# Optimization experiments

Hardware: AMD Instinct MI355X
Metric: run time of the kernel (lower is better)

Reference implementation:

```python
import jax, jax.numpy as jnp
import numpy as np

B, DP, N = 8, 3, 2048
DM, K = 128, 20
C4 = DM // 4


def _gather(pts, idx):
    # pts: (b, n, c), idx: (b, n, k) -> (b, n, k, c)
    return jax.vmap(lambda p, i: p[i])(pts, idx)


def _bn(x, gamma, beta, eps=1e-5):
    # train-mode BatchNorm1d; x: (b, c, n), stats over (batch, points)
    mu = jnp.mean(x, axis=(0, 2), keepdims=True)
    var = jnp.var(x, axis=(0, 2), keepdims=True)
    return gamma[None, :, None] * (x - mu) * jax.lax.rsqrt(var + eps) + beta[None, :, None]


def setup_inputs() -> dict:
    key = jax.random.key(0)
    ks = iter(jax.random.split(key, 32))

    def U(shape):
        s = 1.0 / np.sqrt(shape[-1])
        return jax.random.uniform(next(ks), shape, jnp.float32, -s, s)

    d = {}
    d['features'] = jax.random.normal(next(ks), (B, DP, N), jnp.float32)
    d['fc1_w'] = U((DM, DP)); d['fc1_b'] = U((DM,))
    d['fc2_w'] = U((DM, DM)); d['fc2_b'] = U((DM,))
    d['bn_g'] = jnp.ones((DM,), jnp.float32); d['bn_b'] = jnp.zeros((DM,), jnp.float32)
    d['fb1_w'] = U((DM, 2 * DP)); d['fb1_b'] = U((DM,))
    d['fb2_w'] = U((DM, DM)); d['fb2_b'] = U((DM,))
    d['fg1_w'] = U((DM, DM)); d['fg1_b'] = U((DM,))
    d['fg2_w'] = U((DM, DM)); d['fg2_b'] = U((DM,))
    d['wq'] = U((DM, DM)); d['wk'] = U((DM, DM)); d['wv'] = U((DM, DM))
    d['sa_qk_w'] = U((C4, DM))  # q_conv and k_conv share this weight
    d['sa_v_w'] = U((DM, DM)); d['sa_v_b'] = U((DM,))
    d['sa_t_w'] = U((DM, DM)); d['sa_t_b'] = U((DM,))
    d['sa_bn_g'] = jnp.ones((DM,), jnp.float32); d['sa_bn_b'] = jnp.zeros((DM,), jnp.float32)
    return d


def reference(features, fc1_w, fc1_b, fc2_w, fc2_b, bn_g, bn_b,
              fb1_w, fb1_b, fb2_w, fb2_b, fg1_w, fg1_b, fg2_w, fg2_b,
              wq, wk, wv, sa_qk_w, sa_v_w, sa_v_b, sa_t_w, sa_t_b,
              sa_bn_g, sa_bn_b):
    x = features  # (b, dp, n)
    # --- kNN: negative squared pairwise distance, top-k largest = nearest ---
    inner = -2.0 * jnp.einsum('bdn,bdm->bnm', x, x)
    xx = jnp.sum(x * x, axis=1)  # (b, n)
    pd = -xx[:, :, None] - inner - xx[:, None, :]  # (b, n, n)
    idx = jax.lax.top_k(pd, K)[1]  # (b, n, K) neighbor indices
    # --- get_graph_feature: gather neighbors, concat (nbr - ctr, ctr) ---
    xt = jnp.transpose(x, (0, 2, 1))  # (b, n, dp)
    nbr = _gather(xt, idx)  # (b, n, K, dp)
    ctr = jnp.broadcast_to(xt[:, :, None, :], nbr.shape)
    kf = jnp.concatenate([nbr - ctr, ctr], axis=-1)  # (b, n, K, 2*dp)
    # fb edge MLP
    kf = jax.nn.relu(kf @ fb1_w.T + fb1_b) @ fb2_w.T + fb2_b  # (b, n, K, DM)
    # --- point-transformer attention ---
    x1 = xt @ fc1_w.T + fc1_b  # (b, n, DM)
    q = x1 @ wq.T
    kg = _gather(x1 @ wk.T, idx)  # (b, n, K, DM)
    vg = _gather(x1 @ wv.T, idx)  # (b, n, K, DM)
    a = q[:, :, None, :] - kg + kf
    a = jax.nn.relu(a @ fg1_w.T + fg1_b) @ fg2_w.T + fg2_b  # fc_gamma
    attn = jax.nn.log_softmax(a / jnp.sqrt(jnp.float32(DM)), axis=-2)  # over K
    res = jnp.einsum('bnkf,bnkf->bnf', attn, vg + kf)  # (b, n, DM)
    res = jnp.transpose(res @ fc2_w.T + fc2_b, (0, 2, 1))  # (b, DM, n)
    res = jax.nn.relu(_bn(res, bn_g, bn_b)) + jnp.transpose(x1, (0, 2, 1))
    # --- SA_Layer: offset self-attention (q and k share weights) ---
    xqk = jnp.einsum('cd,bdn->bcn', sa_qk_w, res)  # (b, C4, n)
    energy = jnp.einsum('bcn,bcm->bnm', xqk, xqk)  # (b, n, n)
    att = jax.nn.softmax(energy, axis=-1)
    att = att / (1e-9 + jnp.sum(att, axis=1, keepdims=True))
    xv = jnp.einsum('cd,bdn->bcn', sa_v_w, res) + sa_v_b[None, :, None]
    xr = jnp.einsum('bcn,bnm->bcm', xv, att)  # x_v @ attention
    xr = jnp.einsum('cd,bdn->bcn', sa_t_w, res - xr) + sa_t_b[None, :, None]
    xr = jax.nn.relu(_bn(xr, sa_bn_g, sa_bn_b))
    out = res + xr  # (b, DM, n)
    return (jnp.transpose(out, (0, 2, 1)), attn)
```

## Files before the change

kernel.cpp:

```cpp
#include <hip/hip_runtime.h>

#define NPTS 16384
#define NB 2048
#define KNN 20

typedef __attribute__((ext_vector_type(4))) float f32x4;
typedef __attribute__((ext_vector_type(8))) short short8;

union U4S8 { uint4 q; short8 s; };
union W4   { unsigned u[4]; short8 s; };

__device__ __forceinline__ unsigned bf16_rne(float v){
    unsigned u = __float_as_uint(v);
    return (u + 0x7fffu + ((u>>16)&1u)) >> 16;
}
__device__ __forceinline__ unsigned cvt_pk_bf16(float a, float b){
    unsigned r;
    asm("v_cvt_pk_bf16_f32 %0, %1, %2" : "=v"(r) : "v"(a), "v"(b));
    return r;
}
__device__ __forceinline__ unsigned pack_hl(float v){
    unsigned h = cvt_pk_bf16(v, v);
    float r = v - __uint_as_float(h << 16);
    unsigned l = cvt_pk_bf16(r, r);
    return __builtin_amdgcn_perm(l, h, 0x05040100u);
}
__device__ __forceinline__ void pack2(float v0, float v1, unsigned& h2, unsigned& l2){
    h2 = cvt_pk_bf16(v0, v1);
    float r0 = v0 - __uint_as_float(h2 << 16);
    float r1 = v1 - __uint_as_float(h2 & 0xffff0000u);
    l2 = cvt_pk_bf16(r0, r1);
}
__device__ __forceinline__ void split_hl(uint4 w0, uint4 w1, short8& hi, short8& lo){
    W4 h, l;
    h.u[0] = __builtin_amdgcn_perm(w0.y, w0.x, 0x05040100u);
    l.u[0] = __builtin_amdgcn_perm(w0.y, w0.x, 0x07060302u);
    h.u[1] = __builtin_amdgcn_perm(w0.w, w0.z, 0x05040100u);
    l.u[1] = __builtin_amdgcn_perm(w0.w, w0.z, 0x07060302u);
    h.u[2] = __builtin_amdgcn_perm(w1.y, w1.x, 0x05040100u);
    l.u[2] = __builtin_amdgcn_perm(w1.y, w1.x, 0x07060302u);
    h.u[3] = __builtin_amdgcn_perm(w1.w, w1.z, 0x05040100u);
    l.u[3] = __builtin_amdgcn_perm(w1.w, w1.z, 0x07060302u);
    hi = h.s; lo = l.s;
}
__device__ __forceinline__ f32x4 e3_mfma(short8 Ah, short8 Al, short8 Bh, short8 Bl){
    f32x4 acc = (f32x4){0.f,0.f,0.f,0.f};
    acc = __builtin_amdgcn_mfma_f32_16x16x32_bf16(Al, Bh, acc, 0,0,0);
    acc = __builtin_amdgcn_mfma_f32_16x16x32_bf16(Ah, Bl, acc, 0,0,0);
    acc = __builtin_amdgcn_mfma_f32_16x16x32_bf16(Ah, Bh, acc, 0,0,0);
    return acc;
}

__global__ void transpose_kernel(const float* in, float* out, int C){
    int gid = blockIdx.x*256 + threadIdx.x;
    if (gid >= 128*C) return;
    int j = gid / C, c = gid - j*C;
    out[gid] = in[c*128 + j];
}

__global__ void pack_bfrag_kernel(const float* w0, const float* w1, const float* w2, unsigned short* out){
    int gid = blockIdx.x*256 + threadIdx.x;
    if (gid >= 3*16384) return;
    int m = gid >> 14, r = gid & 16383;
    const float* W = (m==0)?w0:(m==1)?w1:w2;
    int e = r & 7, lane = (r>>3) & 63, ks = (r>>9)&3, ct = r>>11;
    int c = ct*16 + (lane&15), j = ks*32 + (lane>>4)*8 + e;
    out[gid] = (unsigned short)bf16_rne(W[c*128 + j]);
}

__global__ __launch_bounds__(256) void knn_kernel(const float* feat, int* g_idx){
    __shared__ float sx[2048], sy[2048], sz[2048];
    __shared__ int swin[32*20];
    int tid = threadIdx.x;
    int p0 = blockIdx.x * 32;
    int b = p0 >> 11;
    const float* fb = feat + b*3*2048;
    for (int i = tid; i < 2048; i += 256){ sx[i]=fb[i]; sy[i]=fb[2048+i]; sz[i]=fb[4096+i]; }
    __syncthreads();

    int chunk = tid & 7, pl = tid >> 3;
    int n = (p0 + pl) & 2047;
    double xi = sx[n], yi = sy[n], zi = sz[n];

    const double SENT = __longlong_as_double(0x7FE0000000000000ll);
    double val[20];
#pragma unroll
    for (int k=0;k<20;k++) val[k] = SENT;

    int base = chunk*256;
    for (int ii=0; ii<256; ii++){
        int i = (ii + (chunk<<2)) & 255;
        int j = base + i;
        double dx = (double)sx[j]-xi, dy = (double)sy[j]-yi, dz = (double)sz[j]-zi;
        double d2 = dx*dx + dy*dy + dz*dz;
        long long kb = ((__double_as_longlong(d2) & ~2047ll) | (long long)j) + (1ll<<61);
        double key = __longlong_as_double(kb);
#pragma unroll
        for (int s=19; s>=1; s--)
            val[s] = fmax(val[s-1], fmin(val[s], key));
        val[0] = fmin(val[0], key);
    }

    for (int kk=0; kk<20; kk++){
        double h = val[0];
        h = fmin(h, __shfl_xor(h, 1));
        h = fmin(h, __shfl_xor(h, 2));
        h = fmin(h, __shfl_xor(h, 4));
        if (val[0] == h){
            swin[pl*20 + kk] = (int)(__double_as_longlong(h) & 2047ll);
#pragma unroll
            for (int s=0;s<19;s++) val[s] = val[s+1];
            val[19] = SENT;
        }
    }
    __syncthreads();
    for (int t = tid; t < 640; t += 256)
        g_idx[p0*20 + t] = swin[t];
}

__global__ void x1_kernel(const float* feat, const float* w, const float* bias, float* x1){
    int gid = blockIdx.x*256 + threadIdx.x;
    int p = gid >> 7, c = gid & 127;
    int b = p >> 11, n = p & 2047;
    const float* fb = feat + b*6144 + n;
    float v = bias[c];
    v += w[c*3+0]*fb[0];
    v += w[c*3+1]*fb[2048];
    v += w[c*3+2]*fb[4096];
    x1[gid] = v;
}

__global__ __launch_bounds__(256) void qkv_kernel(const float* x1, const float* wqT, const float* wkT,
                                                  const float* wvT, float* q, float* k1, float* v1){
    __shared__ float sx[16][128];
    int tid = threadIdx.x;
    int p0 = blockIdx.x * 16;
    for (int t = tid; t < 2048; t += 256) sx[t>>7][t&127] = x1[p0*128 + t];
    __syncthreads();
    int cg = tid & 31, pg = tid >> 5, c0 = cg*4;
    float aq[2][4] = {{0,0,0,0},{0,0,0,0}};
    float ak[2][4] = {{0,0,0,0},{0,0,0,0}};
    float av[2][4] = {{0,0,0,0},{0,0,0,0}};
    for (int j=0;j<128;j++){
        float xa = sx[pg][j], xb = sx[pg+8][j];
        float4 wq4 = *(const float4*)&wqT[j*128 + c0];
        float4 wk4 = *(const float4*)&wkT[j*128 + c0];
        float4 wv4 = *(const float4*)&wvT[j*128 + c0];
        const float* wqp = &wq4.x; const float* wkp = &wk4.x; const float* wvp = &wv4.x;
#pragma unroll
        for (int ci=0; ci<4; ci++){
            aq[0][ci] += wqp[ci]*xa; aq[1][ci] += wqp[ci]*xb;
            ak[0][ci] += wkp[ci]*xa; ak[1][ci] += wkp[ci]*xb;
            av[0][ci] += wvp[ci]*xa; av[1][ci] += wvp[ci]*xb;
        }
    }
#pragma unroll
    for (int pp=0; pp<2; pp++){
        int p = p0 + pg + pp*8;
        *(float4*)&q [p*128 + c0] = make_float4(aq[pp][0],aq[pp][1],aq[pp][2],aq[pp][3]);
        *(float4*)&k1[p*128 + c0] = make_float4(ak[pp][0],ak[pp][1],ak[pp][2],ak[pp][3]);
        *(float4*)&v1[p*128 + c0] = make_float4(av[pp][0],av[pp][1],av[pp][2],av[pp][3]);
    }
}

#define ASTR 136
__device__ __forceinline__ void stage_gemm(const unsigned short* bH, const unsigned short* bL,
                                           const unsigned short* wb, int lane, int ct0, f32x4 acc[5][2]){
    short8 bf[2][4];
#pragma unroll
    for (int ci=0; ci<2; ci++)
#pragma unroll
    for (int ks=0; ks<4; ks++){
        U4S8 u; u.q = *(const uint4*)(wb + ((ct0+ci)*4 + ks)*512 + lane*8);
        bf[ci][ks] = u.s;
    }
#pragma unroll
    for (int rt=0; rt<5; rt++)
#pragma unroll
    for (int ci=0; ci<2; ci++)
        acc[rt][ci] = (f32x4){0.f,0.f,0.f,0.f};
    int abase = (lane&15)*ASTR + (lane>>4)*8;
#pragma unroll
    for (int rt=0; rt<5; rt++){
#pragma unroll
        for (int ks=0; ks<4; ks++){
            int off = rt*16*ASTR + ks*32 + abase;
            short8 hi = *(const short8*)(bH + off);
            short8 lo = *(const short8*)(bL + off);
#pragma unroll
            for (int ci=0; ci<2; ci++){
                acc[rt][ci] = __builtin_amdgcn_mfma_f32_16x16x32_bf16(hi, bf[ci][ks], acc[rt][ci], 0,0,0);
                acc[rt][ci] = __builtin_amdgcn_mfma_f32_16x16x32_bf16(lo, bf[ci][ks], acc[rt][ci], 0,0,0);
            }
        }
    }
}

__device__ __forceinline__ void store4(unsigned short* bH, unsigned short* bL,
                                       int r0, int col, unsigned h2, unsigned l2, unsigned h3, unsigned l3){
    bH[(r0+0)*ASTR + col] = (unsigned short)h2;        bL[(r0+0)*ASTR + col] = (unsigned short)l2;
    bH[(r0+1)*ASTR + col] = (unsigned short)(h2>>16);  bL[(r0+1)*ASTR + col] = (unsigned short)(l2>>16);
    bH[(r0+2)*ASTR + col] = (unsigned short)h3;        bL[(r0+2)*ASTR + col] = (unsigned short)l3;
    bH[(r0+3)*ASTR + col] = (unsigned short)(h3>>16);  bL[(r0+3)*ASTR + col] = (unsigned short)(l3>>16);
}

__global__ __launch_bounds__(256, 3) void attn_kernel(
        const float* feat, const int* g_idx, const float* g_q, const float* g_k1, const float* g_v1,
        const unsigned short* wpk,
        const float* fb1w, const float* fb1b, const float* fb2b, const float* fg1b, const float* fg2b,
        float* g_attn, float* g_res){
    __shared__ __align__(16) unsigned short bufH[80*ASTR];
    __shared__ __align__(16) unsigned short bufL[80*ASTR];
    __shared__ float sh_q[512];
    __shared__ float sh_e[80*6];
    __shared__ int   sh_ix[80];
    int tid = threadIdx.x;
    int lane = tid & 63, wave = tid >> 6;
    int bidx = blockIdx.x;
    int blk = ((bidx & 7) << 9) | (bidx >> 3);
    int gp0 = blk * 4;
    int b = gp0 >> 11;
    size_t kvbase = (size_t)b*2048*128;

    sh_q[tid]     = g_q[gp0*128 + tid];
    sh_q[tid+256] = g_q[gp0*128 + tid + 256];
    if (tid < 80){
        int r = tid;
        int nb = g_idx[gp0*20 + r];
        sh_ix[r] = nb;
        int p = (r*205) >> 12;
        int n = (gp0 & 2047) + p;
        const float* fbp = feat + b*6144;
        float cx = fbp[n], cy = fbp[2048+n], cz = fbp[4096+n];
        float nx = fbp[nb], ny = fbp[2048+nb], nz = fbp[4096+nb];
        sh_e[r*6+0] = nx-cx; sh_e[r*6+1] = ny-cy; sh_e[r*6+2] = nz-cz;
        sh_e[r*6+3] = cx;    sh_e[r*6+4] = cy;    sh_e[r*6+5] = cz;
    }
    __syncthreads();

    {
        int c = tid & 127, rh = tid >> 7;
        float w0=fb1w[c*6+0], w1=fb1w[c*6+1], w2=fb1w[c*6+2], w3=fb1w[c*6+3], w4=fb1w[c*6+4], w5=fb1w[c*6+5];
        float bb = fb1b[c];
#pragma unroll
        for (int t=0; t<20; t++){
            int r0 = t*4 + rh, r1 = r0 + 2;
            const float* e0 = &sh_e[r0*6];
            const float* e1 = &sh_e[r1*6];
            float v0 = fmaxf(bb + w0*e0[0]+w1*e0[1]+w2*e0[2]+w3*e0[3]+w4*e0[4]+w5*e0[5], 0.f);
            float v1 = fmaxf(bb + w0*e1[0]+w1*e1[1]+w2*e1[2]+w3*e1[3]+w4*e1[4]+w5*e1[5], 0.f);
            unsigned h2, l2; pack2(v0, v1, h2, l2);
            bufH[r0*ASTR + c] = (unsigned short)h2;       bufL[r0*ASTR + c] = (unsigned short)l2;
            bufH[r1*ASTR + c] = (unsigned short)(h2>>16); bufL[r1*ASTR + c] = (unsigned short)(l2>>16);
        }
    }
    __syncthreads();

    int ct0 = wave*2;
    int colA = ct0*16 + (lane&15);
    int colB = colA + 16;
    int quad = lane >> 4;
    f32x4 acc[5][2];
    float kfr[5][2][4];

    stage_gemm(bufH, bufL, wpk, lane, ct0, acc);
    {
        float bA = fb2b[colA], bB = fb2b[colB];
#pragma unroll
        for (int rt=0; rt<5; rt++)
#pragma unroll
        for (int ci=0; ci<2; ci++){
            int col = ci ? colB : colA;
            float bias = ci ? bB : bA;
            float ain[4];
#pragma unroll
            for (int reg=0; reg<4; reg++){
                int row = rt*16 + quad*4 + reg;
                float kf = acc[rt][ci][reg] + bias;
                kfr[rt][ci][reg] = kf;
                int p = (row*205)>>12;
                int nb = sh_ix[row];
                float kg = g_k1[kvbase + (size_t)nb*128 + col];
                ain[reg] = sh_q[p*128 + col] - kg + kf;
            }
            unsigned h2,l2,h3,l3;
            pack2(ain[0], ain[1], h2, l2);
            pack2(ain[2], ain[3], h3, l3);
            acc[rt][ci][0] = __uint_as_float(h2); acc[rt][ci][1] = __uint_as_float(l2);
            acc[rt][ci][2] = __uint_as_float(h3); acc[rt][ci][3] = __uint_as_float(l3);
        }
    }
    __syncthreads();
#pragma unroll
    for (int rt=0; rt<5; rt++)
#pragma unroll
    for (int ci=0; ci<2; ci++)
        store4(bufH, bufL, rt*16 + quad*4, ci ? colB : colA,
               __float_as_uint(acc[rt][ci][0]), __float_as_uint(acc[rt][ci][1]),
               __float_as_uint(acc[rt][ci][2]), __float_as_uint(acc[rt][ci][3]));
    __syncthreads();

    stage_gemm(bufH, bufL, wpk + 16384, lane, ct0, acc);
    {
        float bA = fg1b[colA], bB = fg1b[colB];
#pragma unroll
        for (int rt=0; rt<5; rt++)
#pragma unroll
        for (int ci=0; ci<2; ci++){
            float bias = ci ? bB : bA;
            float v0 = fmaxf(acc[rt][ci][0] + bias, 0.f);
            float v1 = fmaxf(acc[rt][ci][1] + bias, 0.f);
            float v2 = fmaxf(acc[rt][ci][2] + bias, 0.f);
            float v3 = fmaxf(acc[rt][ci][3] + bias, 0.f);
            unsigned h2,l2,h3,l3;
            pack2(v0, v1, h2, l2);
            pack2(v2, v3, h3, l3);
            acc[rt][ci][0] = __uint_as_float(h2); acc[rt][ci][1] = __uint_as_float(l2);
            acc[rt][ci][2] = __uint_as_float(h3); acc[rt][ci][3] = __uint_as_float(l3);
        }
    }
    __syncthreads();
#pragma unroll
    for (int rt=0; rt<5; rt++)
#pragma unroll
    for (int ci=0; ci<2; ci++)
        store4(bufH, bufL, rt*16 + quad*4, ci ? colB : colA,
               __float_as_uint(acc[rt][ci][0]), __float_as_uint(acc[rt][ci][1]),
               __float_as_uint(acc[rt][ci][2]), __float_as_uint(acc[rt][ci][3]));
    __syncthreads();

    stage_gemm(bufH, bufL, wpk + 32768, lane, ct0, acc);
    {
        const float SCALE = 0.08838834764831845f;
        const float NEGF  = -3e38f;
        float bA = fg2b[colA], bB = fg2b[colB];
#pragma unroll
        for (int ci=0; ci<2; ci++){
            int col = ci ? colB : colA;
            float bias = ci ? bB : bA;
            float lm[5];
#pragma unroll
            for (int rt=0; rt<5; rt++){
#pragma unroll
                for (int reg=0; reg<4; reg++)
                    acc[rt][ci][reg] = (acc[rt][ci][reg] + bias) * SCALE;
                lm[rt] = fmaxf(fmaxf(acc[rt][ci][0], acc[rt][ci][1]), fmaxf(acc[rt][ci][2], acc[rt][ci][3]));
            }
            float m[4];
#pragma unroll
            for (int j=0; j<4; j++){
                float c1 = (j<=quad) ? lm[j]   : NEGF;
                float c2 = (j>=quad) ? lm[j+1] : NEGF;
                m[j] = fmaxf(c1, c2);
                m[j] = fmaxf(m[j], __shfl_xor(m[j], 16));
                m[j] = fmaxf(m[j], __shfl_xor(m[j], 32));
            }
            float mp[5];
            mp[0] = m[0];
            mp[1] = (1<=quad) ? m[1] : m[0];
            mp[2] = (2<=quad) ? m[2] : m[1];
            mp[3] = (3<=quad) ? m[3] : m[2];
            mp[4] = m[3];
            float ls[5];
#pragma unroll
            for (int rt=0; rt<5; rt++){
                float e0 = expf(acc[rt][ci][0] - mp[rt]);
                float e1 = expf(acc[rt][ci][1] - mp[rt]);
                float e2 = expf(acc[rt][ci][2] - mp[rt]);
                float e3 = expf(acc[rt][ci][3] - mp[rt]);
                ls[rt] = (e0 + e1) + (e2 + e3);
            }
            float L[4];
#pragma unroll
            for (int j=0; j<4; j++){
                float c1 = (j<=quad) ? ls[j]   : 0.f;
                float c2 = (j>=quad) ? ls[j+1] : 0.f;
                float S = c1 + c2;
                S += __shfl_xor(S, 16);
                S += __shfl_xor(S, 32);
                L[j] = m[j] + logf(S);
            }
            float Lp[5];
            Lp[0] = L[0];
            Lp[1] = (1<=quad) ? L[1] : L[0];
            Lp[2] = (2<=quad) ? L[2] : L[1];
            Lp[3] = (3<=quad) ? L[3] : L[2];
            Lp[4] = L[3];
            float pv[5];
#pragma unroll
            for (int rt=0; rt<5; rt++){
                float pacc = 0.f;
#pragma unroll
                for (int reg=0; reg<4; reg++){
                    int row = rt*16 + quad*4 + reg;
                    float at = acc[rt][ci][reg] - Lp[rt];
                    g_attn[(size_t)(gp0*20 + row)*128 + col] = at;
                    int nb = sh_ix[row];
                    float vv = g_v1[kvbase + (size_t)nb*128 + col];
                    pacc += at * (vv + kfr[rt][ci][reg]);
                }
                pv[rt] = pacc;
            }
#pragma unroll
            for (int j=0; j<4; j++){
                float c1 = (j<=quad) ? pv[j]   : 0.f;
                float c2 = (j>=quad) ? pv[j+1] : 0.f;
                float P = c1 + c2;
                P += __shfl_xor(P, 16);
                P += __shfl_xor(P, 32);
                pv[j] = P;
            }
            float rv = (quad==0) ? pv[0] : (quad==1) ? pv[1] : (quad==2) ? pv[2] : pv[3];
            g_res[(size_t)(gp0 + quad)*128 + col] = rv;
        }
    }
}

__global__ __launch_bounds__(256) void lin_kernel(const float* X, const float* WT, const float* bias, float* Y){
    __shared__ float sx[16][128];
    int tid = threadIdx.x;
    int p0 = blockIdx.x * 16;
    for (int t = tid; t < 2048; t += 256) sx[t>>7][t&127] = X[p0*128 + t];
    __syncthreads();
    int cg = tid & 31, pg = tid >> 5, c0 = cg*4;
    float a[2][4] = {{0,0,0,0},{0,0,0,0}};
    for (int j=0;j<128;j++){
        float xa = sx[pg][j], xb = sx[pg+8][j];
        float4 w4 = *(const float4*)&WT[j*128 + c0];
        const float* wp = &w4.x;
#pragma unroll
        for (int ci=0;ci<4;ci++){ a[0][ci] += wp[ci]*xa; a[1][ci] += wp[ci]*xb; }
    }
    float4 bv = *(const float4*)&bias[c0];
    const float* bp = &bv.x;
#pragma unroll
    for (int pp=0;pp<2;pp++){
        int p = p0 + pg + pp*8;
        *(float4*)&Y[p*128+c0] = make_float4(a[pp][0]+bp[0], a[pp][1]+bp[1], a[pp][2]+bp[2], a[pp][3]+bp[3]);
    }
}

__global__ __launch_bounds__(256) void l6_kernel(const float* Xa, const float* Xb, const float* WT,
                                                 const float* bias, float* Y){
    __shared__ float sx[16][128];
    int tid = threadIdx.x;
    int p0 = blockIdx.x * 16;
    for (int t = tid; t < 2048; t += 256) sx[t>>7][t&127] = Xa[p0*128 + t] - Xb[p0*128 + t];
    __syncthreads();
    int cg = tid & 31, pg = tid >> 5, c0 = cg*4;
    float a[2][4] = {{0,0,0,0},{0,0,0,0}};
    for (int j=0;j<128;j++){
        float xa = sx[pg][j], xb = sx[pg+8][j];
        float4 w4 = *(const float4*)&WT[j*128 + c0];
        const float* wp = &w4.x;
#pragma unroll
        for (int ci=0;ci<4;ci++){ a[0][ci] += wp[ci]*xa; a[1][ci] += wp[ci]*xb; }
    }
    float4 bv = *(const float4*)&bias[c0];
    const float* bp = &bv.x;
#pragma unroll
    for (int pp=0;pp<2;pp++){
        int p = p0 + pg + pp*8;
        *(float4*)&Y[p*128+c0] = make_float4(a[pp][0]+bp[0], a[pp][1]+bp[1], a[pp][2]+bp[2], a[pp][3]+bp[3]);
    }
}

__global__ __launch_bounds__(256) void l5_kernel(const float* X, const float* WvT, const float* vb,
                                                 const float* WqkT, unsigned* xvt_pk, unsigned* xqk_pk){
    __shared__ float sx[16][128];
    int tid = threadIdx.x;
    int p0 = blockIdx.x * 16;
    for (int t = tid; t < 2048; t += 256) sx[t>>7][t&127] = X[p0*128 + t];
    __syncthreads();
    int cg = tid & 31, pg = tid >> 5, c0 = cg*4;
    {
        float a[2][4] = {{0,0,0,0},{0,0,0,0}};
        for (int j=0;j<128;j++){
            float xa = sx[pg][j], xb = sx[pg+8][j];
            float4 w4 = *(const float4*)&WvT[j*128 + c0];
            const float* wp = &w4.x;
#pragma unroll
            for (int ci=0;ci<4;ci++){ a[0][ci] += wp[ci]*xa; a[1][ci] += wp[ci]*xb; }
        }
        float4 bv = *(const float4*)&vb[c0];
        const float* bp = &bv.x;
#pragma unroll
        for (int pp=0;pp<2;pp++){
            int p = p0 + pg + pp*8;
            int bb = p >> 11, n = p & 2047;
            unsigned* dst = xvt_pk + ((size_t)(bb*64 + (n>>5)))*4096 + (n&31);
#pragma unroll
            for (int ci=0;ci<4;ci++) dst[(c0+ci)*32] = pack_hl(a[pp][ci] + bp[ci]);
        }
    }
    if (cg < 8){
        int cq = cg*4;
        float a[2][4] = {{0,0,0,0},{0,0,0,0}};
        for (int j=0;j<128;j++){
            float xa = sx[pg][j], xb = sx[pg+8][j];
            float4 w4 = *(const float4*)&WqkT[j*32 + cq];
            const float* wp = &w4.x;
#pragma unroll
            for (int ci=0;ci<4;ci++){ a[0][ci] += wp[ci]*xa; a[1][ci] += wp[ci]*xb; }
        }
#pragma unroll
        for (int pp=0;pp<2;pp++){
            int p = p0 + pg + pp*8;
            uint4 w;
            w.x = pack_hl(a[pp][0]); w.y = pack_hl(a[pp][1]);
            w.z = pack_hl(a[pp][2]); w.w = pack_hl(a[pp][3]);
            *(uint4*)&xqk_pk[p*32 + cq] = w;
        }
    }
}

__global__ void bn_stats_kernel(const float* X, float* sums){
    int tid = threadIdx.x;
    int c = tid & 127, half = tid >> 7;
    int r0 = blockIdx.x*128 + half*64;
    float s = 0.f, sq = 0.f;
    for (int r = r0; r < r0+64; r++){
        float v = X[r*128 + c];
        s += v; sq += v*v;
    }
    atomicAdd(&sums[c], s);
    atomicAdd(&sums[128+c], sq);
}

__global__ void bn1_apply_kernel(const float* res2, const float* x1, const float* sums,
                                 const float* g, const float* beta, float* sres){
    int gid = blockIdx.x*256 + threadIdx.x;
    int c = gid & 127;
    float mu = sums[c] * (1.0f/16384.f);
    float var = sums[128+c] * (1.0f/16384.f) - mu*mu;
    float inv = 1.0f / sqrtf(var + 1e-5f);
    float y = g[c]*(res2[gid]-mu)*inv + beta[c];
    sres[gid] = fmaxf(y, 0.f) + x1[gid];
}

__global__ void final_kernel(const float* sres, const float* xr2, const float* sums,
                             const float* g, const float* beta, float* out0){
    int gid = blockIdx.x*256 + threadIdx.x;
    int c = gid & 127;
    float mu = sums[c] * (1.0f/16384.f);
    float var = sums[128+c] * (1.0f/16384.f) - mu*mu;
    float inv = 1.0f / sqrtf(var + 1e-5f);
    float y = g[c]*(xr2[gid]-mu)*inv + beta[c];
    out0[gid] = sres[gid] + fmaxf(y, 0.f);
}

__global__ __launch_bounds__(256) void sa_stats_kernel(const unsigned* xqk_pk, float* rm, float* irs){
    int tid = threadIdx.x;
    int lane = tid & 63, wave = tid >> 6;
    int b = blockIdx.x & 7;
    int i0 = (blockIdx.x >> 3) * 64 + wave*16;
    const unsigned* qb = xqk_pk + (size_t)b*2048*32;
    int quad = lane >> 4, l15 = lane & 15;
    const unsigned* ap = qb + (i0 + l15)*32 + quad*8;
    uint4 a0 = *(const uint4*)ap, a1 = *(const uint4*)(ap+4);
    short8 Ah, Al; split_hl(a0, a1, Ah, Al);

    float m[4] = {-3e38f,-3e38f,-3e38f,-3e38f};
    for (int jt=0; jt<128; jt++){
        const unsigned* bp = qb + (jt*16 + l15)*32 + quad*8;
        uint4 b0 = *(const uint4*)bp, b1 = *(const uint4*)(bp+4);
        short8 Bh, Bl; split_hl(b0,b1,Bh,Bl);
        f32x4 e = (f32x4){0.f,0.f,0.f,0.f};
        e = __builtin_amdgcn_mfma_f32_16x16x32_bf16(Ah, Bh, e, 0,0,0);
#pragma unroll
        for (int r=0;r<4;r++) m[r] = fmaxf(m[r], e[r]);
    }
#pragma unroll
    for (int mk=1; mk<16; mk<<=1)
#pragma unroll
        for (int r=0;r<4;r++) m[r] = fmaxf(m[r], __shfl_xor(m[r], mk));

    float s[4] = {0.f,0.f,0.f,0.f};
    for (int jt=0; jt<128; jt++){
        const unsigned* bp = qb + (jt*16 + l15)*32 + quad*8;
        uint4 b0 = *(const uint4*)bp, b1 = *(const uint4*)(bp+4);
        short8 Bh, Bl; split_hl(b0,b1,Bh,Bl);
        f32x4 e = e3_mfma(Ah,Al,Bh,Bl);
#pragma unroll
        for (int r=0;r<4;r++) s[r] += expf(e[r]-m[r]);
    }
#pragma unroll
    for (int mk=1; mk<16; mk<<=1)
#pragma unroll
        for (int r=0;r<4;r++) s[r] += __shfl_xor(s[r], mk);
    if (l15 == 0){
#pragma unroll
        for (int r=0;r<4;r++){
            int row = i0 + quad*4 + r;
            rm[b*2048+row]  = m[r];
            irs[b*2048+row] = 1.0f/s[r];
        }
    }
}

#define SXV_STR 36
#define ATT_STR 36
#define NSPLIT 4
__global__ __launch_bounds__(256) void sa_xr_part_kernel(const unsigned* xqk_pk, const unsigned* xvt_pk,
                                                         const float* rm, const float* irs,
                                                         float* part, float* cspart){
    __shared__ __align__(16) unsigned sxv[128*SXV_STR];
    __shared__ __align__(16) unsigned attT[32*ATT_STR];
    __shared__ float scs[2][2][16];
    int tid = threadIdx.x;
    int lane = tid & 63, wave = tid >> 6;
    int quad = lane >> 4, l15 = lane & 15;
    int bid = blockIdx.x;
    int b   = bid & 7;
    int rest = bid >> 3;
    int ns  = rest >> 6;
    int mt  = rest & 63;
    int m0 = mt*32;
    int rt = wave >> 1, ct = wave & 1;
    const unsigned* qb = xqk_pk + (size_t)b*2048*32;

    short8 Bmh, Bml;
    {
        const unsigned* bp = qb + (m0 + ct*16 + l15)*32 + quad*8;
        uint4 b0 = *(const uint4*)bp, b1 = *(const uint4*)(bp+4);
        split_hl(b0,b1,Bmh,Bml);
    }
    f32x4 acc[4];
#pragma unroll
    for (int cc=0;cc<4;cc++) acc[cc] = (f32x4){0.f,0.f,0.f,0.f};
    float cs_acc = 0.f;

    int ch0 = ns*16;
    for (int ci16=0; ci16<16; ci16++){
        int chunk = ch0 + ci16;
        int n0 = chunk*32;
        __syncthreads();
        const unsigned* src = xvt_pk + ((size_t)(b*64 + chunk))*4096;
#pragma unroll
        for (int it=0; it<4; it++){
            int u = tid + it*256;
            int c = u >> 3, part_ = u & 7;
            *(uint4*)&sxv[c*SXV_STR + part_*4] = *(const uint4*)(src + u*4);
        }
        const unsigned* ap = qb + (n0 + rt*16 + l15)*32 + quad*8;
        uint4 a0 = *(const uint4*)ap, a1 = *(const uint4*)(ap+4);
        short8 Ah, Al; split_hl(a0,a1,Ah,Al);
        f32x4 e = e3_mfma(Ah,Al,Bmh,Bml);
#pragma unroll
        for (int r=0;r<4;r++){
            int rowg = b*2048 + n0 + rt*16 + quad*4 + r;
            float att = expf(e[r] - rm[rowg]) * irs[rowg];
            cs_acc += att;
            attT[(ct*16+l15)*ATT_STR + rt*16 + quad*4 + r] = pack_hl(att);
        }
        __syncthreads();
        const unsigned* arp = attT + (ct*16+l15)*ATT_STR + quad*8;
        uint4 aa0 = *(const uint4*)arp, aa1 = *(const uint4*)(arp+4);
        short8 Aph, Apl; split_hl(aa0,aa1,Aph,Apl);
#pragma unroll
        for (int cc=0; cc<4; cc++){
            int c0 = (rt*4 + cc)*16;
            const unsigned* xp = &sxv[(c0 + l15)*SXV_STR + quad*8];
            uint4 x0 = *(const uint4*)xp, x1 = *(const uint4*)(xp+4);
            short8 Xh, Xl; split_hl(x0,x1,Xh,Xl);
            acc[cc] = __builtin_amdgcn_mfma_f32_16x16x32_bf16(Apl, Xh, acc[cc], 0,0,0);
            acc[cc] = __builtin_amdgcn_mfma_f32_16x16x32_bf16(Aph, Xl, acc[cc], 0,0,0);
            acc[cc] = __builtin_amdgcn_mfma_f32_16x16x32_bf16(Aph, Xh, acc[cc], 0,0,0);
        }
    }
    cs_acc += __shfl_xor(cs_acc, 16);
    cs_acc += __shfl_xor(cs_acc, 32);
    if (lane < 16) scs[ct][rt][lane] = cs_acc;
    __syncthreads();
    if (tid < 32)
        cspart[(size_t)(ns*8 + b)*2048 + m0 + tid] = scs[tid>>4][0][tid&15] + scs[tid>>4][1][tid&15];
#pragma unroll
    for (int cc=0; cc<4; cc++){
        int c0 = (rt*4 + cc)*16;
#pragma unroll
        for (int r=0;r<4;r++){
            int mloc = ct*16 + quad*4 + r;
            part[((size_t)(ns*8 + b)*2048 + m0 + mloc)*128 + c0 + l15] = acc[cc][r];
        }
    }
}

__global__ void sa_combine_kernel(const float* part, const float* cspart, float* xr){
    int gid = blockIdx.x*256 + threadIdx.x;
    int bm = gid >> 7;
    float cs = cspart[bm] + cspart[bm+16384] + cspart[bm+2*16384] + cspart[bm+3*16384];
    float v  = part[gid] + part[gid+2097152] + part[gid+2*2097152] + part[gid+3*2097152];
    xr[gid] = v * (1.0f/(1e-9f + cs));
}

extern "C" void kernel_launch(void* const* d_in, const int* in_sizes, int n_in,
                              void* d_out, int out_size, void* d_ws, size_t ws_size,
                              hipStream_t stream){
    (void)in_sizes; (void)n_in; (void)out_size; (void)ws_size;
    const float* feat = (const float*)d_in[0];
    const float* fc1w = (const float*)d_in[1];  const float* fc1b = (const float*)d_in[2];
    const float* fc2w = (const float*)d_in[3];  const float* fc2b = (const float*)d_in[4];
    const float* bng  = (const float*)d_in[5];  const float* bnb  = (const float*)d_in[6];
    const float* fb1w = (const float*)d_in[7];  const float* fb1b = (const float*)d_in[8];
    const float* fb2w = (const float*)d_in[9];  const float* fb2b = (const float*)d_in[10];
    const float* fg1w = (const float*)d_in[11]; const float* fg1b = (const float*)d_in[12];
    const float* fg2w = (const float*)d_in[13]; const float* fg2b = (const float*)d_in[14];
    const float* wq   = (const float*)d_in[15]; const float* wk   = (const float*)d_in[16];
    const float* wv   = (const float*)d_in[17];
    const float* saqk = (const float*)d_in[18];
    const float* savw = (const float*)d_in[19]; const float* savb = (const float*)d_in[20];
    const float* satw = (const float*)d_in[21]; const float* satb = (const float*)d_in[22];
    const float* sabng= (const float*)d_in[23]; const float* sabnb= (const float*)d_in[24];

    float* out0 = (float*)d_out;
    float* out1 = out0 + 2097152;

    char* ws = (char*)d_ws;
    size_t off = 0;
    auto A = [&](size_t bytes)->char*{
        char* r = ws + off;
        off = (off + bytes + 255) & ~(size_t)255;
        return r;
    };
    const size_t PBUF = (size_t)NPTS*128*4;
    int*      g_idx  = (int*)A((size_t)NPTS*KNN*4);
    float*    g_x1   = (float*)A(PBUF);
    float*    g_q    = (float*)A(PBUF);
    float*    g_k1   = (float*)A(PBUF);
    float*    g_v1   = (float*)A(PBUF);
    float*    g_res  = (float*)A(PBUF);
    float*    g_res2 = (float*)A(PBUF);
    float*    g_sres = (float*)A(PBUF);
    float*    g_xr   = (float*)A(PBUF);
    float*    g_xr2  = (float*)A(PBUF);
    unsigned* g_xvt_pk = (unsigned*)A((size_t)NPTS*128*4);
    unsigned* g_xqk_pk = (unsigned*)A((size_t)NPTS*32*4);
    float*    g_rm   = (float*)A((size_t)NPTS*4);
    float*    g_rs   = (float*)A((size_t)NPTS*4);
    float*    g_stats= (float*)A((size_t)512*4);
    unsigned short* g_wpk = (unsigned short*)A((size_t)3*16384*2);
    float*    g_wqT  = (float*)A(65536);
    float*    g_wkT  = (float*)A(65536);
    float*    g_wvT  = (float*)A(65536);
    float*    g_fc2T = (float*)A(65536);
    float*    g_savT = (float*)A(65536);
    float*    g_satT = (float*)A(65536);
    float*    g_sqkT = (float*)A(16384);

    float* bn1s = g_stats;
    float* bn2s = g_stats + 256;

    float* g_part   = g_q;
    float* g_cspart = g_res2;

    hipMemsetAsync(g_stats, 0, (size_t)512*4, stream);

    pack_bfrag_kernel<<<192, 256, 0, stream>>>(fb2w, fg1w, fg2w, g_wpk);
    transpose_kernel<<<64, 256, 0, stream>>>(wq,   g_wqT, 128);
    transpose_kernel<<<64, 256, 0, stream>>>(wk,   g_wkT, 128);
    transpose_kernel<<<64, 256, 0, stream>>>(wv,   g_wvT, 128);
    transpose_kernel<<<64, 256, 0, stream>>>(fc2w, g_fc2T, 128);
    transpose_kernel<<<64, 256, 0, stream>>>(savw, g_savT, 128);
    transpose_kernel<<<64, 256, 0, stream>>>(satw, g_satT, 128);
    transpose_kernel<<<16, 256, 0, stream>>>(saqk, g_sqkT, 32);

    knn_kernel<<<512, 256, 0, stream>>>(feat, g_idx);
    x1_kernel<<<8192, 256, 0, stream>>>(feat, fc1w, fc1b, g_x1);
    qkv_kernel<<<1024, 256, 0, stream>>>(g_x1, g_wqT, g_wkT, g_wvT, g_q, g_k1, g_v1);
    attn_kernel<<<4096, 256, 0, stream>>>(feat, g_idx, g_q, g_k1, g_v1, g_wpk,
                                          fb1w, fb1b, fb2b, fg1b, fg2b, out1, g_res);
    lin_kernel<<<1024, 256, 0, stream>>>(g_res, g_fc2T, fc2b, g_res2);
    bn_stats_kernel<<<128, 256, 0, stream>>>(g_res2, bn1s);
    bn1_apply_kernel<<<8192, 256, 0, stream>>>(g_res2, g_x1, bn1s, bng, bnb, g_sres);
    l5_kernel<<<1024, 256, 0, stream>>>(g_sres, g_savT, savb, g_sqkT, g_xvt_pk, g_xqk_pk);
    sa_stats_kernel<<<256, 256, 0, stream>>>(g_xqk_pk, g_rm, g_rs);
    sa_xr_part_kernel<<<512*NSPLIT, 256, 0, stream>>>(g_xqk_pk, g_xvt_pk, g_rm, g_rs, g_part, g_cspart);
    sa_combine_kernel<<<8192, 256, 0, stream>>>(g_part, g_cspart, g_xr);
    l6_kernel<<<1024, 256, 0, stream>>>(g_sres, g_xr, g_satT, satb, g_xr2);
    bn_stats_kernel<<<128, 256, 0, stream>>>(g_xr2, bn2s);
    final_kernel<<<8192, 256, 0, stream>>>(g_sres, g_xr2, bn2s, sabng, sabnb, out0);
}
```

Measured before the change: 773.2 us.

## Stage attn output through LDS for coalesced stores; split sa_stats over waves

In attn_kernel the attention weights are first written into a shared buffer that reuses the bufH/bufL space, then copied out with coalesced float4 stores instead of scattered per-column global writes. Occupancy hint drops from 3 to 2 blocks per CU. Separately, sa_stats_kernel now has each block handle 16 rows, with the four waves splitting the column range and combining the max and sum through shared memory, and the launch grows fourfold to raise parallelism. This adds extra barriers and shared-memory traffic.

```diff
diff --git a/kernel.cpp b/kernel.cpp
--- a/kernel.cpp
+++ b/kernel.cpp
@@ -164,6 +164,7 @@
 }
 
 #define ASTR 136
+#define ATB_STR 132
 __device__ __forceinline__ void stage_gemm(const unsigned short* bH, const unsigned short* bL,
                                            const unsigned short* wb, int lane, int ct0, f32x4 acc[5][2]){
     short8 bf[2][4];
@@ -204,13 +205,15 @@
     bH[(r0+3)*ASTR + col] = (unsigned short)(h3>>16);  bL[(r0+3)*ASTR + col] = (unsigned short)(l3>>16);
 }
 
-__global__ __launch_bounds__(256, 3) void attn_kernel(
+__global__ __launch_bounds__(256, 2) void attn_kernel(
         const float* feat, const int* g_idx, const float* g_q, const float* g_k1, const float* g_v1,
         const unsigned short* wpk,
         const float* fb1w, const float* fb1b, const float* fb2b, const float* fg1b, const float* fg2b,
         float* g_attn, float* g_res){
-    __shared__ __align__(16) unsigned short bufH[80*ASTR];
-    __shared__ __align__(16) unsigned short bufL[80*ASTR];
+    __shared__ __align__(16) unsigned char smem[80*ASTR*2*2];
+    unsigned short* bufH = (unsigned short*)smem;
+    unsigned short* bufL = (unsigned short*)smem + 80*ASTR;
+    float* atb = (float*)smem;
     __shared__ float sh_q[512];
     __shared__ float sh_e[80*6];
     __shared__ int   sh_ix[80];
@@ -330,6 +333,7 @@
     __syncthreads();
 
     stage_gemm(bufH, bufL, wpk + 32768, lane, ct0, acc);
+    __syncthreads();
     {
         const float SCALE = 0.08838834764831845f;
         const float NEGF  = -3e38f;
@@ -394,7 +398,7 @@
                 for (int reg=0; reg<4; reg++){
                     int row = rt*16 + quad*4 + reg;
                     float at = acc[rt][ci][reg] - Lp[rt];
-                    g_attn[(size_t)(gp0*20 + row)*128 + col] = at;
+                    atb[row*ATB_STR + col] = at;
                     int nb = sh_ix[row];
                     float vv = g_v1[kvbase + (size_t)nb*128 + col];
                     pacc += at * (vv + kfr[rt][ci][reg]);
@@ -414,6 +418,16 @@
             g_res[(size_t)(gp0 + quad)*128 + col] = rv;
         }
     }
+    __syncthreads();
+    {
+        float* gat = g_attn + (size_t)gp0*20*128;
+#pragma unroll
+        for (int k2=0; k2<10; k2++){
+            int n = tid + k2*256;
+            int row = n >> 5, c4 = (n & 31)*4;
+            *(float4*)&gat[row*128 + c4] = *(const float4*)&atb[row*ATB_STR + c4];
+        }
+    }
 }
 
 __global__ __launch_bounds__(256) void lin_kernel(const float* X, const float* WT, const float* bias, float* Y){
@@ -550,18 +564,21 @@
 }
 
 __global__ __launch_bounds__(256) void sa_stats_kernel(const unsigned* xqk_pk, float* rm, float* irs){
+    __shared__ float sred[4][16];
+    __shared__ float srm[16];
     int tid = threadIdx.x;
     int lane = tid & 63, wave = tid >> 6;
     int b = blockIdx.x & 7;
-    int i0 = (blockIdx.x >> 3) * 64 + wave*16;
+    int i0 = (blockIdx.x >> 3) * 16;
     const unsigned* qb = xqk_pk + (size_t)b*2048*32;
     int quad = lane >> 4, l15 = lane & 15;
     const unsigned* ap = qb + (i0 + l15)*32 + quad*8;
     uint4 a0 = *(const uint4*)ap, a1 = *(const uint4*)(ap+4);
     short8 Ah, Al; split_hl(a0, a1, Ah, Al);
 
+    int jt0 = wave*32;
     float m[4] = {-3e38f,-3e38f,-3e38f,-3e38f};
-    for (int jt=0; jt<128; jt++){
+    for (int jt=jt0; jt<jt0+32; jt++){
         const unsigned* bp = qb + (jt*16 + l15)*32 + quad*8;
         uint4 b0 = *(const uint4*)bp, b1 = *(const uint4*)(bp+4);
         short8 Bh, Bl; split_hl(b0,b1,Bh,Bl);
@@ -574,27 +591,41 @@
     for (int mk=1; mk<16; mk<<=1)
 #pragma unroll
         for (int r=0;r<4;r++) m[r] = fmaxf(m[r], __shfl_xor(m[r], mk));
+    if (l15 == 0){
+#pragma unroll
+        for (int r=0;r<4;r++) sred[wave][quad*4+r] = m[r];
+    }
+    __syncthreads();
+    if (tid < 16)
+        srm[tid] = fmaxf(fmaxf(sred[0][tid], sred[1][tid]), fmaxf(sred[2][tid], sred[3][tid]));
+    __syncthreads();
+    float mp[4];
+#pragma unroll
+    for (int r=0;r<4;r++) mp[r] = srm[quad*4+r];
 
     float s[4] = {0.f,0.f,0.f,0.f};
-    for (int jt=0; jt<128; jt++){
+    for (int jt=jt0; jt<jt0+32; jt++){
         const unsigned* bp = qb + (jt*16 + l15)*32 + quad*8;
         uint4 b0 = *(const uint4*)bp, b1 = *(const uint4*)(bp+4);
         short8 Bh, Bl; split_hl(b0,b1,Bh,Bl);
         f32x4 e = e3_mfma(Ah,Al,Bh,Bl);
 #pragma unroll
-        for (int r=0;r<4;r++) s[r] += expf(e[r]-m[r]);
+        for (int r=0;r<4;r++) s[r] += expf(e[r]-mp[r]);
     }
 #pragma unroll
     for (int mk=1; mk<16; mk<<=1)
 #pragma unroll
         for (int r=0;r<4;r++) s[r] += __shfl_xor(s[r], mk);
+    __syncthreads();
     if (l15 == 0){
 #pragma unroll
-        for (int r=0;r<4;r++){
-            int row = i0 + quad*4 + r;
-            rm[b*2048+row]  = m[r];
-            irs[b*2048+row] = 1.0f/s[r];
-        }
+        for (int r=0;r<4;r++) sred[wave][quad*4+r] = s[r];
+    }
+    __syncthreads();
+    if (tid < 16){
+        float S = (sred[0][tid] + sred[1][tid]) + (sred[2][tid] + sred[3][tid]);
+        rm[b*2048 + i0 + tid]  = srm[tid];
+        irs[b*2048 + i0 + tid] = 1.0f/S;
     }
 }
 
@@ -773,7 +804,7 @@
     bn_stats_kernel<<<128, 256, 0, stream>>>(g_res2, bn1s);
     bn1_apply_kernel<<<8192, 256, 0, stream>>>(g_res2, g_x1, bn1s, bng, bnb, g_sres);
     l5_kernel<<<1024, 256, 0, stream>>>(g_sres, g_savT, savb, g_sqkT, g_xvt_pk, g_xqk_pk);
-    sa_stats_kernel<<<256, 256, 0, stream>>>(g_xqk_pk, g_rm, g_rs);
+    sa_stats_kernel<<<1024, 256, 0, stream>>>(g_xqk_pk, g_rm, g_rs);
     sa_xr_part_kernel<<<512*NSPLIT, 256, 0, stream>>>(g_xqk_pk, g_xvt_pk, g_rm, g_rs, g_part, g_cspart);
     sa_combine_kernel<<<8192, 256, 0, stream>>>(g_part, g_cspart, g_xr);
     l6_kernel<<<1024, 256, 0, stream>>>(g_sres, g_xr, g_satT, satb, g_xr2);
```

After: 763.7 us. No clear change (-1.2%).
